# Performance work log

Measured on AMD Instinct MI355X. Metric: run time of the kernel, lower is better.

The kernel has to match this reference:

```python
import jax, jax.numpy as jnp
import numpy as np

# Model dims
P_SPECS = [(6, 256), (7, 256)]          # pattern_length -> num_patterns (ordered)
P = 512                                  # total_num_patterns
MAXL = 7                                 # max_pattern_length
ND = 2                                   # num_diags (self-loop diag + main diag)
D = 300                                  # embedding_dim
V = 50000                                # vocab size
B = 32                                   # batch size
T = 128                                  # max_doc_len
NC = 2                                   # num_classes
NEG = -1e30                              # max-sum semiring zero; one = 0.0
END_STATES = np.concatenate([np.full(n, l - 1, dtype=np.int32) for l, n in P_SPECS])


def setup_inputs() -> dict:
    key = jax.random.key(0)
    ks = jax.random.split(key, 8)
    tokens = jax.random.randint(ks[0], (B, T), 0, V, dtype=jnp.int32)
    doc_lens = jax.random.randint(ks[1], (B,), 64, T + 1, dtype=jnp.int32)
    emb_table = jax.random.normal(ks[2], (V, D), dtype=jnp.float32)
    diags = jax.random.normal(ks[3], (P * ND * MAXL, D), dtype=jnp.float32)
    diags = diags / jnp.linalg.norm(diags, axis=1, keepdims=True)  # normalize(diags)
    bias = jax.random.normal(ks[4], (P * ND * MAXL, 1), dtype=jnp.float32)
    epsilons = jax.random.normal(ks[5], (P, MAXL - 1), dtype=jnp.float32)
    bn_weight = jnp.ones((P,), jnp.float32)
    bn_bias = jnp.zeros((P,), jnp.float32)
    final_w = 0.05 * jax.random.normal(ks[6], (NC, P), dtype=jnp.float32)
    final_b = jnp.zeros((NC,), jnp.float32)
    return dict(tokens=tokens, doc_lens=doc_lens, emb_table=emb_table, diags=diags,
                bias=bias, epsilons=epsilons, bn_weight=bn_weight, bn_bias=bn_bias,
                final_w=final_w, final_b=final_b)


def reference(tokens, doc_lens, emb_table, diags, bias, epsilons,
              bn_weight, bn_bias, final_w, final_b):
    # --- transition matrices (max-sum semiring: from_outer is identity) ---
    emb = emb_table[tokens]                                   # [B,T,D]
    # mm(diags, embeddings) + bias_scale * bias  (bias_scale = 1.0)
    ts = jnp.einsum('btd,kd->btk', emb, diags) + bias[:, 0]   # [B,T,P*ND*MAXL]
    ts = ts.reshape(B, T, P, ND, MAXL)                        # [B,T,P,ND,MAXL]

    end = jnp.asarray(END_STATES)                             # [P]
    hid0 = jnp.full((B, P, MAXL), NEG, jnp.float32).at[:, :, 0].set(0.0)
    sc0 = jnp.full((B, P), NEG, jnp.float32)                  # semiring.zero
    zpad = jnp.full((B, P, 1), NEG, jnp.float32)              # zero_padding
    rpad = jnp.zeros((B, P, 1), jnp.float32)                  # restart_padding (one)

    # epsilon_values = epsilon_scale (one=0) + epsilons
    def step(carry, xs):
        hid, sc = carry
        tm, i = xs                                            # tm: [B,P,ND,MAXL]
        # epsilon transitions
        ae = jnp.maximum(hid, jnp.concatenate([zpad, hid[:, :, :-1] + epsilons], axis=2))
        # main path: diag index -1 (the main diagonal)
        main = jnp.concatenate([rpad, ae[:, :, :-1] + tm[:, :, -1, :-1]], axis=2)
        # self loops: diag 0, self_loop_scale = semiring.one = 0
        sl = ae + tm[:, :, 0, :]
        hid = jnp.maximum(main, sl)
        endv = jnp.take_along_axis(hid, jnp.broadcast_to(end[None, :, None], (B, P, 1)), axis=2)[:, :, 0]
        sc = jnp.where((doc_lens > i)[:, None], jnp.maximum(sc, endv), sc)
        return (hid, sc), None

    (_, scores), _ = jax.lax.scan(step, (hid0, sc0),
                                  (jnp.moveaxis(ts, 1, 0), jnp.arange(T, dtype=jnp.int32)))

    # BatchNorm1d (training mode: biased batch statistics)
    mean = scores.mean(axis=0)
    var = scores.var(axis=0)
    scores = (scores - mean) * jax.lax.rsqrt(var + 1e-5) * bn_weight + bn_bias
    # binarize_scores
    scores = jnp.sign(jax.nn.relu(scores))
    # final linear layer
    return scores @ final_w.T + final_b                       # [B, NC]
```

## Files before the change

kernel.cpp:

```cpp
#include <hip/hip_runtime.h>

#define BB 32
#define TT 128
#define PP 512
#define DD 300
#define NPK 7168
#define KP 320
#define NEG -1e30f

typedef _Float16 half8 __attribute__((ext_vector_type(8)));
typedef _Float16 half4 __attribute__((ext_vector_type(4)));
typedef float floatx4 __attribute__((ext_vector_type(4)));

__device__ __forceinline__ void async_load16(const void* g, void* l) {
    __builtin_amdgcn_global_load_lds(
        (const __attribute__((address_space(1))) void*)g,
        (__attribute__((address_space(3))) void*)l, 16, 0, 0);
}

__device__ __forceinline__ floatx4 mfma16(half8 a, half8 b, floatx4 c) {
    return __builtin_amdgcn_mfma_f32_16x16x32_f16(a, b, c, 0, 0, 0);
}

__global__ __launch_bounds__(256) void pack_a_kernel(
    const int* __restrict__ tokens, const float* __restrict__ emb,
    _Float16* __restrict__ Ah, _Float16* __restrict__ Al)
{
    const int idx = blockIdx.x * 256 + threadIdx.x;
    if (idx >= 4096 * 80) return;
    const int m = idx / 80;
    const int c = idx - m * 80;
    float4 x = make_float4(0.f, 0.f, 0.f, 0.f);
    if (c < 75) x = *(const float4*)(emb + (size_t)tokens[m] * DD + c * 4);
    half4 h, l;
    h.x = (_Float16)x.x; l.x = (_Float16)((x.x - (float)h.x) * 4096.f);
    h.y = (_Float16)x.y; l.y = (_Float16)((x.y - (float)h.y) * 4096.f);
    h.z = (_Float16)x.z; l.z = (_Float16)((x.z - (float)h.z) * 4096.f);
    h.w = (_Float16)x.w; l.w = (_Float16)((x.w - (float)h.w) * 4096.f);
    *(half4*)(Ah + (size_t)m * KP + c * 4) = h;
    *(half4*)(Al + (size_t)m * KP + c * 4) = l;
}

__global__ __launch_bounds__(256) void pack_b_kernel(
    const float* __restrict__ diags,
    _Float16* __restrict__ Bh, _Float16* __restrict__ Bl)
{
    const int idx = blockIdx.x * 256 + threadIdx.x;
    if (idx >= NPK * 80) return;
    const int n = idx / 80;
    const int c = idx - n * 80;
    float4 x = make_float4(0.f, 0.f, 0.f, 0.f);
    if (c < 75) x = *(const float4*)(diags + (size_t)n * DD + c * 4);
    half4 h, l;
    h.x = (_Float16)x.x; l.x = (_Float16)((x.x - (float)h.x) * 4096.f);
    h.y = (_Float16)x.y; l.y = (_Float16)((x.y - (float)h.y) * 4096.f);
    h.z = (_Float16)x.z; l.z = (_Float16)((x.z - (float)h.z) * 4096.f);
    h.w = (_Float16)x.w; l.w = (_Float16)((x.w - (float)h.w) * 4096.f);
    *(half4*)(Bh + (size_t)n * KP + c * 4) = h;
    *(half4*)(Bl + (size_t)n * KP + c * 4) = l;
}

__global__ __launch_bounds__(256, 2) void gemm_f16_kernel(
    const _Float16* __restrict__ Ah, const _Float16* __restrict__ Al,
    const _Float16* __restrict__ Bh, const _Float16* __restrict__ Bl,
    const float* __restrict__ bias, float* __restrict__ C)
{
    __shared__ __align__(16) _Float16 AsH[128 * 32];
    __shared__ __align__(16) _Float16 AsL[128 * 32];
    __shared__ __align__(16) _Float16 BsH[128 * 32];
    __shared__ __align__(16) _Float16 BsL[128 * 32];

    const int tid = threadIdx.x;
    const int w = tid >> 6, ln = tid & 63;
    const int n0 = blockIdx.x * 128, m0 = blockIdx.y * 128;
    const int wm = w & 1, wn = w >> 1;

    floatx4 acc0[4][4], acc1[4][4];
    #pragma unroll
    for (int i = 0; i < 4; ++i)
        #pragma unroll
        for (int j = 0; j < 4; ++j) {
            acc0[i][j] = (floatx4){0.f, 0.f, 0.f, 0.f};
            acc1[i][j] = (floatx4){0.f, 0.f, 0.f, 0.f};
        }

    const int lrow = ln >> 2;
    const int lkc  = ln & 3;
    const int fr   = ln & 15;
    const int kg   = ln >> 4;

    for (int kt = 0; kt < KP / 32; ++kt) {
        const int k0 = kt * 32;
        #pragma unroll
        for (int s = 0; s < 2; ++s) {
            const int r0 = (w * 2 + s) * 16;
            const int row = r0 + lrow;
            const size_t ga = (size_t)(m0 + row) * KP + k0 + lkc * 8;
            const size_t gb = (size_t)(n0 + row) * KP + k0 + lkc * 8;
            async_load16(Ah + ga, &AsH[r0 * 32]);
            async_load16(Al + ga, &AsL[r0 * 32]);
            async_load16(Bh + gb, &BsH[r0 * 32]);
            async_load16(Bl + gb, &BsL[r0 * 32]);
        }
        __syncthreads();

        half8 a_h[4], a_l[4];
        #pragma unroll
        for (int i = 0; i < 4; ++i) {
            const int off = (wm * 64 + i * 16 + fr) * 32 + kg * 8;
            a_h[i] = *(const half8*)&AsH[off];
            a_l[i] = *(const half8*)&AsL[off];
        }
        #pragma unroll
        for (int j = 0; j < 4; ++j) {
            const int off = (wn * 64 + j * 16 + fr) * 32 + kg * 8;
            const half8 b_h = *(const half8*)&BsH[off];
            const half8 b_l = *(const half8*)&BsL[off];
            #pragma unroll
            for (int i = 0; i < 4; ++i) {
                acc0[i][j] = mfma16(a_h[i], b_h, acc0[i][j]);
                acc1[i][j] = mfma16(a_h[i], b_l, acc1[i][j]);
                acc1[i][j] = mfma16(a_l[i], b_h, acc1[i][j]);
            }
        }
        __syncthreads();
    }

    #pragma unroll
    for (int j = 0; j < 4; ++j) {
        const int n = n0 + wn * 64 + j * 16 + fr;
        const float bj = bias[n];
        #pragma unroll
        for (int i = 0; i < 4; ++i) {
            const int mbase = m0 + wm * 64 + i * 16 + kg * 4;
            #pragma unroll
            for (int r = 0; r < 4; ++r) {
                C[(size_t)(mbase + r) * NPK + n] =
                    acc0[i][j][r] + acc1[i][j][r] * (1.0f / 4096.0f) + bj;
            }
        }
    }
}

__global__ __launch_bounds__(256) void gemm_kernel(
    const int* __restrict__ tokens,
    const float* __restrict__ emb,
    const float* __restrict__ diags,
    const float* __restrict__ bias,
    float* __restrict__ C)
{
    __shared__ __align__(16) float As[16][132];
    __shared__ __align__(16) float Bs[16][132];
    __shared__ int rowbase[128];

    const int tid = threadIdx.x;
    const int n0 = blockIdx.x * 128;
    const int m0 = blockIdx.y * 128;

    if (tid < 128) rowbase[tid] = tokens[m0 + tid] * DD;
    __syncthreads();

    const int tx4 = (tid & 15) * 4;
    const int ty4 = (tid >> 4) * 4;
    const int r0  = tid >> 2;
    const int kq  = (tid & 3) * 4;

    float acc[8][8];
    #pragma unroll
    for (int i = 0; i < 8; ++i)
        #pragma unroll
        for (int j = 0; j < 8; ++j) acc[i][j] = 0.f;

    for (int kk = 0; kk < DD; kk += 16) {
        float4 a0, a1, b0, b1;
        const bool kval = (kk + kq) < DD;
        if (kval) {
            a0 = *(const float4*)(emb + rowbase[r0] + kk + kq);
            a1 = *(const float4*)(emb + rowbase[r0 + 64] + kk + kq);
            b0 = *(const float4*)(diags + (size_t)(n0 + r0) * DD + kk + kq);
            b1 = *(const float4*)(diags + (size_t)(n0 + r0 + 64) * DD + kk + kq);
        } else {
            a0 = make_float4(0.f, 0.f, 0.f, 0.f);
            a1 = a0; b0 = a0; b1 = a0;
        }
        __syncthreads();
        As[kq + 0][r0] = a0.x; As[kq + 1][r0] = a0.y; As[kq + 2][r0] = a0.z; As[kq + 3][r0] = a0.w;
        As[kq + 0][r0 + 64] = a1.x; As[kq + 1][r0 + 64] = a1.y; As[kq + 2][r0 + 64] = a1.z; As[kq + 3][r0 + 64] = a1.w;
        Bs[kq + 0][r0] = b0.x; Bs[kq + 1][r0] = b0.y; Bs[kq + 2][r0] = b0.z; Bs[kq + 3][r0] = b0.w;
        Bs[kq + 0][r0 + 64] = b1.x; Bs[kq + 1][r0 + 64] = b1.y; Bs[kq + 2][r0 + 64] = b1.z; Bs[kq + 3][r0 + 64] = b1.w;
        __syncthreads();
        #pragma unroll
        for (int k = 0; k < 16; ++k) {
            float4 av0 = *(const float4*)&As[k][ty4];
            float4 av1 = *(const float4*)&As[k][ty4 + 64];
            float4 bv0 = *(const float4*)&Bs[k][tx4];
            float4 bv1 = *(const float4*)&Bs[k][tx4 + 64];
            float a[8] = {av0.x, av0.y, av0.z, av0.w, av1.x, av1.y, av1.z, av1.w};
            float b[8] = {bv0.x, bv0.y, bv0.z, bv0.w, bv1.x, bv1.y, bv1.z, bv1.w};
            #pragma unroll
            for (int i = 0; i < 8; ++i)
                #pragma unroll
                for (int j = 0; j < 8; ++j)
                    acc[i][j] = fmaf(a[i], b[j], acc[i][j]);
        }
    }

    const float4 bias0 = *(const float4*)(bias + n0 + tx4);
    const float4 bias1 = *(const float4*)(bias + n0 + 64 + tx4);
    #pragma unroll
    for (int i = 0; i < 8; ++i) {
        const int m = m0 + ((i < 4) ? (ty4 + i) : (64 + ty4 + (i - 4)));
        float4 lo = make_float4(acc[i][0] + bias0.x, acc[i][1] + bias0.y,
                                acc[i][2] + bias0.z, acc[i][3] + bias0.w);
        float4 hi = make_float4(acc[i][4] + bias1.x, acc[i][5] + bias1.y,
                                acc[i][6] + bias1.z, acc[i][7] + bias1.w);
        *(float4*)(C + (size_t)m * NPK + n0 + tx4) = lo;
        *(float4*)(C + (size_t)m * NPK + n0 + 64 + tx4) = hi;
    }
}

__global__ __launch_bounds__(64) void scan_kernel(
    const float* __restrict__ ts,
    const float* __restrict__ epsilons,
    const int* __restrict__ doc_lens,
    float* __restrict__ scores)
{
    const int b = blockIdx.x;
    const int p = blockIdx.y * 64 + threadIdx.x;
    const int dl = doc_lens[b];

    float e[6];
    #pragma unroll
    for (int i = 0; i < 6; ++i) e[i] = epsilons[p * 6 + i];

    const float* base = ts + (size_t)b * TT * NPK + p * 14;

    float h0 = 0.f, h1 = NEG, h2 = NEG, h3 = NEG, h4 = NEG, h5 = NEG, h6 = NEG;
    float sc = NEG;
    const bool end5 = (p < 256);

    float buf[4][14];

    auto load = [&](int slot, int t) {
        const float2* s = (const float2*)(base + (size_t)t * NPK);
        #pragma unroll
        for (int i = 0; i < 7; ++i) ((float2*)buf[slot])[i] = s[i];
    };
    auto step = [&](int slot, int t) {
        const float* tm = buf[slot];
        float ae0 = h0;
        float ae1 = fmaxf(h1, h0 + e[0]);
        float ae2 = fmaxf(h2, h1 + e[1]);
        float ae3 = fmaxf(h3, h2 + e[2]);
        float ae4 = fmaxf(h4, h3 + e[3]);
        float ae5 = fmaxf(h5, h4 + e[4]);
        float ae6 = fmaxf(h6, h5 + e[5]);
        h0 = fmaxf(0.f,          ae0 + tm[0]);
        h1 = fmaxf(ae0 + tm[7],  ae1 + tm[1]);
        h2 = fmaxf(ae1 + tm[8],  ae2 + tm[2]);
        h3 = fmaxf(ae2 + tm[9],  ae3 + tm[3]);
        h4 = fmaxf(ae3 + tm[10], ae4 + tm[4]);
        h5 = fmaxf(ae4 + tm[11], ae5 + tm[5]);
        h6 = fmaxf(ae5 + tm[12], ae6 + tm[6]);
        const float endv = end5 ? h5 : h6;
        if (t < dl) sc = fmaxf(sc, endv);
    };

    #pragma unroll
    for (int j = 0; j < 4; ++j) load(j, j);

    for (int tb = 0; tb < TT - 4; tb += 4) {
        #pragma unroll
        for (int j = 0; j < 4; ++j) {
            step(j, tb + j);
            load(j, tb + j + 4);
        }
    }
    #pragma unroll
    for (int j = 0; j < 4; ++j) step(j, TT - 4 + j);

    scores[p * BB + b] = sc;
}

__global__ __launch_bounds__(512) void finalize_kernel(
    const float* __restrict__ scores,
    const float* __restrict__ bn_w,
    const float* __restrict__ bn_b,
    const float* __restrict__ fw,
    const float* __restrict__ fb,
    float* __restrict__ out)
{
    __shared__ float acc[64];
    const int p = threadIdx.x;
    if (p < 64) acc[p] = 0.f;
    __syncthreads();

    float x[32];
    const float4* sp = (const float4*)(scores + p * 32);
    #pragma unroll
    for (int i = 0; i < 8; ++i) ((float4*)x)[i] = sp[i];

    float mean = 0.f;
    #pragma unroll
    for (int i = 0; i < 32; ++i) mean += x[i];
    mean *= (1.f / 32.f);
    float var = 0.f;
    #pragma unroll
    for (int i = 0; i < 32; ++i) { const float d = x[i] - mean; var = fmaf(d, d, var); }
    var *= (1.f / 32.f);

    const float scale = (1.f / sqrtf(var + 1e-5f)) * bn_w[p];
    const float shift = bn_b[p];
    const float w0 = fw[p], w1 = fw[PP + p];

    for (int b = 0; b < 32; ++b) {
        const float v = (x[b] - mean) * scale + shift;
        const bool bin = v > 0.f;
        float v0 = bin ? w0 : 0.f;
        float v1 = bin ? w1 : 0.f;
        #pragma unroll
        for (int o = 32; o; o >>= 1) {
            v0 += __shfl_xor(v0, o);
            v1 += __shfl_xor(v1, o);
        }
        if ((threadIdx.x & 63) == 0) {
            atomicAdd(&acc[b * 2 + 0], v0);
            atomicAdd(&acc[b * 2 + 1], v1);
        }
    }
    __syncthreads();
    if (p < 64) out[p] = acc[p] + fb[p & 1];
}

extern "C" void kernel_launch(void* const* d_in, const int* in_sizes, int n_in,
                              void* d_out, int out_size, void* d_ws, size_t ws_size,
                              hipStream_t stream) {
    const int*   tokens   = (const int*)d_in[0];
    const int*   doc_lens = (const int*)d_in[1];
    const float* emb      = (const float*)d_in[2];
    const float* diags    = (const float*)d_in[3];
    const float* bias     = (const float*)d_in[4];
    const float* eps      = (const float*)d_in[5];
    const float* bnw      = (const float*)d_in[6];
    const float* bnb      = (const float*)d_in[7];
    const float* fw       = (const float*)d_in[8];
    const float* fb       = (const float*)d_in[9];
    float* out = (float*)d_out;

    float* ts     = (float*)d_ws;
    float* scores = ts + (size_t)4096 * NPK;
    _Float16* Ah  = (_Float16*)(scores + PP * BB);
    _Float16* Al  = Ah + (size_t)4096 * KP;
    _Float16* Bh  = Al + (size_t)4096 * KP;
    _Float16* Bl  = Bh + (size_t)NPK * KP;
    const size_t needed = (size_t)((char*)(Bl + (size_t)NPK * KP) - (char*)d_ws);

    if (ws_size >= needed) {
        pack_a_kernel<<<1280, 256, 0, stream>>>(tokens, emb, Ah, Al);
        pack_b_kernel<<<2240, 256, 0, stream>>>(diags, Bh, Bl);
        gemm_f16_kernel<<<dim3(56, 32), 256, 0, stream>>>(Ah, Al, Bh, Bl, bias, ts);
    } else {
        gemm_kernel<<<dim3(56, 32), 256, 0, stream>>>(tokens, emb, diags, bias, ts);
    }
    scan_kernel<<<dim3(32, 8), 64, 0, stream>>>(ts, eps, doc_lens, scores);
    finalize_kernel<<<1, 512, 0, stream>>>(scores, bnw, bnb, fw, fb, out);
}
```

Measured before the change: 215.8 us.

## Fuse split-f16 GEMM with max-sum scan via LDS tile per batch

The GEMM is retiled so that each block computes all 128 timesteps of one document against 112 columns, which is exactly 8 patterns of 14 transitions. The tile goes into LDS, and 8 lanes then run the recurrence directly from it. This removes the large ts round trip through global memory and the separate scan kernel launch. The cost is that the serial 128-step scan now runs on only 8 lanes per block while the rest of the block sits idle, and the fallback scan loses its software prefetch.

```diff
diff --git a/kernel.cpp b/kernel.cpp
--- a/kernel.cpp
+++ b/kernel.cpp
@@ -6,6 +6,7 @@
 #define DD 300
 #define NPK 7168
 #define KP 320
+#define NT 112
 #define NEG -1e30f
 
 typedef _Float16 half8 __attribute__((ext_vector_type(8)));
@@ -60,26 +61,35 @@
     *(half4*)(Bl + (size_t)n * KP + c * 4) = l;
 }
 
-__global__ __launch_bounds__(256, 2) void gemm_f16_kernel(
+__global__ __launch_bounds__(256, 2) void fused_kernel(
     const _Float16* __restrict__ Ah, const _Float16* __restrict__ Al,
     const _Float16* __restrict__ Bh, const _Float16* __restrict__ Bl,
-    const float* __restrict__ bias, float* __restrict__ C)
-{
-    __shared__ __align__(16) _Float16 AsH[128 * 32];
-    __shared__ __align__(16) _Float16 AsL[128 * 32];
-    __shared__ __align__(16) _Float16 BsH[128 * 32];
-    __shared__ __align__(16) _Float16 BsL[128 * 32];
+    const float* __restrict__ bias,
+    const float* __restrict__ epsilons,
+    const int* __restrict__ doc_lens,
+    float* __restrict__ scores)
+{
+    __shared__ __align__(16) union {
+        struct {
+            _Float16 AsH[128 * 32];
+            _Float16 AsL[128 * 32];
+            _Float16 BsH[NT * 32];
+            _Float16 BsL[NT * 32];
+        } st;
+        float Ct[128][116];
+    } sm;
 
     const int tid = threadIdx.x;
     const int w = tid >> 6, ln = tid & 63;
-    const int n0 = blockIdx.x * 128, m0 = blockIdx.y * 128;
-    const int wm = w & 1, wn = w >> 1;
-
-    floatx4 acc0[4][4], acc1[4][4];
-    #pragma unroll
-    for (int i = 0; i < 4; ++i)
-        #pragma unroll
-        for (int j = 0; j < 4; ++j) {
+    const int b = blockIdx.y;
+    const int n0 = blockIdx.x * NT;
+    const int m0 = b * 128;
+
+    floatx4 acc0[2][7], acc1[2][7];
+    #pragma unroll
+    for (int i = 0; i < 2; ++i)
+        #pragma unroll
+        for (int j = 0; j < 7; ++j) {
             acc0[i][j] = (floatx4){0.f, 0.f, 0.f, 0.f};
             acc1[i][j] = (floatx4){0.f, 0.f, 0.f, 0.f};
         }
@@ -91,54 +101,120 @@
 
     for (int kt = 0; kt < KP / 32; ++kt) {
         const int k0 = kt * 32;
-        #pragma unroll
-        for (int s = 0; s < 2; ++s) {
-            const int r0 = (w * 2 + s) * 16;
-            const int row = r0 + lrow;
-            const size_t ga = (size_t)(m0 + row) * KP + k0 + lkc * 8;
-            const size_t gb = (size_t)(n0 + row) * KP + k0 + lkc * 8;
-            async_load16(Ah + ga, &AsH[r0 * 32]);
-            async_load16(Al + ga, &AsL[r0 * 32]);
-            async_load16(Bh + gb, &BsH[r0 * 32]);
-            async_load16(Bl + gb, &BsL[r0 * 32]);
+        if (w == 0) {
+            #pragma unroll
+            for (int s = 0; s < 8; ++s)
+                async_load16(Ah + (size_t)(m0 + s * 16 + lrow) * KP + k0 + lkc * 8,
+                             &sm.st.AsH[s * 16 * 32]);
+        } else if (w == 1) {
+            #pragma unroll
+            for (int s = 0; s < 8; ++s)
+                async_load16(Al + (size_t)(m0 + s * 16 + lrow) * KP + k0 + lkc * 8,
+                             &sm.st.AsL[s * 16 * 32]);
+        } else if (w == 2) {
+            #pragma unroll
+            for (int s = 0; s < 7; ++s)
+                async_load16(Bh + (size_t)(n0 + s * 16 + lrow) * KP + k0 + lkc * 8,
+                             &sm.st.BsH[s * 16 * 32]);
+        } else {
+            #pragma unroll
+            for (int s = 0; s < 7; ++s)
+                async_load16(Bl + (size_t)(n0 + s * 16 + lrow) * KP + k0 + lkc * 8,
+                             &sm.st.BsL[s * 16 * 32]);
         }
         __syncthreads();
 
-        half8 a_h[4], a_l[4];
-        #pragma unroll
-        for (int i = 0; i < 4; ++i) {
-            const int off = (wm * 64 + i * 16 + fr) * 32 + kg * 8;
-            a_h[i] = *(const half8*)&AsH[off];
-            a_l[i] = *(const half8*)&AsL[off];
-        }
-        #pragma unroll
-        for (int j = 0; j < 4; ++j) {
-            const int off = (wn * 64 + j * 16 + fr) * 32 + kg * 8;
-            const half8 b_h = *(const half8*)&BsH[off];
-            const half8 b_l = *(const half8*)&BsL[off];
-            #pragma unroll
-            for (int i = 0; i < 4; ++i) {
-                acc0[i][j] = mfma16(a_h[i], b_h, acc0[i][j]);
-                acc1[i][j] = mfma16(a_h[i], b_l, acc1[i][j]);
-                acc1[i][j] = mfma16(a_l[i], b_h, acc1[i][j]);
+        half8 ah[2], al[2];
+        #pragma unroll
+        for (int i = 0; i < 2; ++i) {
+            const int off = (w * 32 + i * 16 + fr) * 32 + kg * 8;
+            ah[i] = *(const half8*)&sm.st.AsH[off];
+            al[i] = *(const half8*)&sm.st.AsL[off];
+        }
+        #pragma unroll
+        for (int j = 0; j < 7; ++j) {
+            const int off = (j * 16 + fr) * 32 + kg * 8;
+            const half8 bh = *(const half8*)&sm.st.BsH[off];
+            const half8 bl = *(const half8*)&sm.st.BsL[off];
+            #pragma unroll
+            for (int i = 0; i < 2; ++i) {
+                acc0[i][j] = mfma16(ah[i], bh, acc0[i][j]);
+                acc1[i][j] = mfma16(ah[i], bl, acc1[i][j]);
+                acc1[i][j] = mfma16(al[i], bh, acc1[i][j]);
             }
         }
         __syncthreads();
     }
 
-    #pragma unroll
-    for (int j = 0; j < 4; ++j) {
-        const int n = n0 + wn * 64 + j * 16 + fr;
-        const float bj = bias[n];
-        #pragma unroll
-        for (int i = 0; i < 4; ++i) {
-            const int mbase = m0 + wm * 64 + i * 16 + kg * 4;
-            #pragma unroll
-            for (int r = 0; r < 4; ++r) {
-                C[(size_t)(mbase + r) * NPK + n] =
-                    acc0[i][j][r] + acc1[i][j][r] * (1.0f / 4096.0f) + bj;
-            }
-        }
+    __syncthreads();
+
+    #pragma unroll
+    for (int j = 0; j < 7; ++j) {
+        const int nl = j * 16 + fr;
+        const float bj = bias[n0 + nl];
+        #pragma unroll
+        for (int i = 0; i < 2; ++i) {
+            const int t0 = w * 32 + i * 16 + kg * 4;
+            #pragma unroll
+            for (int r = 0; r < 4; ++r)
+                sm.Ct[t0 + r][nl] = acc0[i][j][r] + acc1[i][j][r] * (1.0f / 4096.0f) + bj;
+        }
+    }
+    __syncthreads();
+
+    if (w == 0 && ln < 8) {
+        const int p = n0 / 14 + ln;
+        const int dl = doc_lens[b];
+        float e0 = epsilons[p * 6 + 0], e1 = epsilons[p * 6 + 1];
+        float e2 = epsilons[p * 6 + 2], e3 = epsilons[p * 6 + 3];
+        float e4 = epsilons[p * 6 + 4], e5 = epsilons[p * 6 + 5];
+        const bool end5 = (p < 256);
+
+        float h0 = 0.f, h1 = NEG, h2 = NEG, h3 = NEG, h4 = NEG, h5 = NEG, h6 = NEG;
+        float sc = NEG;
+        const int co = ln * 14;
+
+        float2 c0, c1, c2, c3, c4, c5, c6;
+        float2 d0, d1, d2, d3, d4, d5, d6;
+
+        #define LOADROW(v0,v1,v2,v3,v4,v5,v6, t) do {            \
+            const float2* _r = (const float2*)&sm.Ct[(t)][co];    \
+            v0=_r[0]; v1=_r[1]; v2=_r[2]; v3=_r[3];               \
+            v4=_r[4]; v5=_r[5]; v6=_r[6]; } while(0)
+
+        #define STEP(v0,v1,v2,v3,v4,v5,v6, t) do {                                 \
+            float ae0 = h0;                                                         \
+            float ae1 = fmaxf(h1, h0 + e0);                                         \
+            float ae2 = fmaxf(h2, h1 + e1);                                         \
+            float ae3 = fmaxf(h3, h2 + e2);                                         \
+            float ae4 = fmaxf(h4, h3 + e3);                                         \
+            float ae5 = fmaxf(h5, h4 + e4);                                         \
+            float ae6 = fmaxf(h6, h5 + e5);                                         \
+            h0 = fmaxf(0.f,           ae0 + v0.x);                                  \
+            h1 = fmaxf(ae0 + v3.y,    ae1 + v0.y);                                  \
+            h2 = fmaxf(ae1 + v4.x,    ae2 + v1.x);                                  \
+            h3 = fmaxf(ae2 + v4.y,    ae3 + v1.y);                                  \
+            h4 = fmaxf(ae3 + v5.x,    ae4 + v2.x);                                  \
+            h5 = fmaxf(ae4 + v5.y,    ae5 + v2.y);                                  \
+            h6 = fmaxf(ae5 + v6.x,    ae6 + v3.x);                                  \
+            const float endv = end5 ? h5 : h6;                                      \
+            if ((t) < dl) sc = fmaxf(sc, endv); } while(0)
+
+        LOADROW(c0,c1,c2,c3,c4,c5,c6, 0);
+        for (int t = 0; t < TT - 2; t += 2) {
+            LOADROW(d0,d1,d2,d3,d4,d5,d6, t + 1);
+            STEP(c0,c1,c2,c3,c4,c5,c6, t);
+            LOADROW(c0,c1,c2,c3,c4,c5,c6, t + 2);
+            STEP(d0,d1,d2,d3,d4,d5,d6, t + 1);
+        }
+        LOADROW(d0,d1,d2,d3,d4,d5,d6, TT - 1);
+        STEP(c0,c1,c2,c3,c4,c5,c6, TT - 2);
+        STEP(d0,d1,d2,d3,d4,d5,d6, TT - 1);
+
+        #undef LOADROW
+        #undef STEP
+
+        scores[p * BB + b] = sc;
     }
 }
 
@@ -196,12 +272,12 @@
             float4 bv0 = *(const float4*)&Bs[k][tx4];
             float4 bv1 = *(const float4*)&Bs[k][tx4 + 64];
             float a[8] = {av0.x, av0.y, av0.z, av0.w, av1.x, av1.y, av1.z, av1.w};
-            float b[8] = {bv0.x, bv0.y, bv0.z, bv0.w, bv1.x, bv1.y, bv1.z, bv1.w};
+            float bb[8] = {bv0.x, bv0.y, bv0.z, bv0.w, bv1.x, bv1.y, bv1.z, bv1.w};
             #pragma unroll
             for (int i = 0; i < 8; ++i)
                 #pragma unroll
                 for (int j = 0; j < 8; ++j)
-                    acc[i][j] = fmaf(a[i], b[j], acc[i][j]);
+                    acc[i][j] = fmaf(a[i], bb[j], acc[i][j]);
         }
     }
 
@@ -239,15 +315,11 @@
     float sc = NEG;
     const bool end5 = (p < 256);
 
-    float buf[4][14];
-
-    auto load = [&](int slot, int t) {
-        const float2* s = (const float2*)(base + (size_t)t * NPK);
-        #pragma unroll
-        for (int i = 0; i < 7; ++i) ((float2*)buf[slot])[i] = s[i];
-    };
-    auto step = [&](int slot, int t) {
-        const float* tm = buf[slot];
+    for (int t = 0; t < TT; ++t) {
+        const float* tm = base + (size_t)t * NPK;
+        float v[14];
+        #pragma unroll
+        for (int i = 0; i < 7; ++i) ((float2*)v)[i] = ((const float2*)tm)[i];
         float ae0 = h0;
         float ae1 = fmaxf(h1, h0 + e[0]);
         float ae2 = fmaxf(h2, h1 + e[1]);
@@ -255,30 +327,16 @@
         float ae4 = fmaxf(h4, h3 + e[3]);
         float ae5 = fmaxf(h5, h4 + e[4]);
         float ae6 = fmaxf(h6, h5 + e[5]);
-        h0 = fmaxf(0.f,          ae0 + tm[0]);
-        h1 = fmaxf(ae0 + tm[7],  ae1 + tm[1]);
-        h2 = fmaxf(ae1 + tm[8],  ae2 + tm[2]);
-        h3 = fmaxf(ae2 + tm[9],  ae3 + tm[3]);
-        h4 = fmaxf(ae3 + tm[10], ae4 + tm[4]);
-        h5 = fmaxf(ae4 + tm[11], ae5 + tm[5]);
-        h6 = fmaxf(ae5 + tm[12], ae6 + tm[6]);
+        h0 = fmaxf(0.f,          ae0 + v[0]);
+        h1 = fmaxf(ae0 + v[7],   ae1 + v[1]);
+        h2 = fmaxf(ae1 + v[8],   ae2 + v[2]);
+        h3 = fmaxf(ae2 + v[9],   ae3 + v[3]);
+        h4 = fmaxf(ae3 + v[10],  ae4 + v[4]);
+        h5 = fmaxf(ae4 + v[11],  ae5 + v[5]);
+        h6 = fmaxf(ae5 + v[12],  ae6 + v[6]);
         const float endv = end5 ? h5 : h6;
         if (t < dl) sc = fmaxf(sc, endv);
-    };
-
-    #pragma unroll
-    for (int j = 0; j < 4; ++j) load(j, j);
-
-    for (int tb = 0; tb < TT - 4; tb += 4) {
-        #pragma unroll
-        for (int j = 0; j < 4; ++j) {
-            step(j, tb + j);
-            load(j, tb + j + 4);
-        }
-    }
-    #pragma unroll
-    for (int j = 0; j < 4; ++j) step(j, TT - 4 + j);
-
+    }
     scores[p * BB + b] = sc;
 }
 
@@ -358,10 +416,11 @@
     if (ws_size >= needed) {
         pack_a_kernel<<<1280, 256, 0, stream>>>(tokens, emb, Ah, Al);
         pack_b_kernel<<<2240, 256, 0, stream>>>(diags, Bh, Bl);
-        gemm_f16_kernel<<<dim3(56, 32), 256, 0, stream>>>(Ah, Al, Bh, Bl, bias, ts);
+        fused_kernel<<<dim3(64, 32), 256, 0, stream>>>(Ah, Al, Bh, Bl, bias, eps,
+                                                       doc_lens, scores);
     } else {
         gemm_kernel<<<dim3(56, 32), 256, 0, stream>>>(tokens, emb, diags, bias, ts);
-    }
-    scan_kernel<<<dim3(32, 8), 64, 0, stream>>>(ts, eps, doc_lens, scores);
+        scan_kernel<<<dim3(32, 8), 64, 0, stream>>>(ts, eps, doc_lens, scores);
+    }
     finalize_kernel<<<1, 512, 0, stream>>>(scores, bnw, bnb, fw, fb, out);
 }
```

Measured after the change: 255.8 us. 18.6% more time.
